# Optimization experiments

Hardware: AMD Instinct MI355X
Metric: run time of the kernel (lower is better)

## Reference

```python
import jax, jax.numpy as jnp
import numpy as np

D, H, L, N, BINS, V = 256, 8, 4, 512, 64, 20
DFF = 4 * D
DH = D // H
LAMBDA_RG = 10.0
STEPS = 10


def _lin(x, W, b):
    # torch nn.Linear convention: W is [out, in]
    return jnp.einsum('...i,oi->...o', x, W) + b


def _ln(x, g, b, eps=1e-5):
    m = x.mean(-1, keepdims=True)
    v = ((x - m) ** 2).mean(-1, keepdims=True)
    return (x - m) / jnp.sqrt(v + eps) * g + b


def _gelu(x):
    return jax.nn.gelu(x, approximate=False)  # torch nn.GELU default = exact erf


def _pos_encoding():
    pos = jnp.arange(N, dtype=jnp.float32)[:, None]
    div = jnp.exp(jnp.arange(0, D, 2, dtype=jnp.float32) * (-np.log(10000.0) / D))
    pe = jnp.zeros((N, D), jnp.float32)
    pe = pe.at[:, 0::2].set(jnp.sin(pos * div))
    pe = pe.at[:, 1::2].set(jnp.cos(pos * div))
    return pe


def _encoder_layer(x, Wqkv, bqkv, Wo, bo, g1, b1n, W1, b1, W2, b2, g2, b2n):
    # post-norm TransformerEncoderLayer, relu FFN, dropout=0 (eval)
    B, n, _ = x.shape
    qkv = _lin(x, Wqkv, bqkv)
    q, k, v = jnp.split(qkv, 3, axis=-1)
    hd = lambda t: t.reshape(B, n, H, DH).transpose(0, 2, 1, 3)
    q, k, v = hd(q), hd(k), hd(v)
    scores = jnp.einsum('bhqd,bhkd->bhqk', q, k) / jnp.sqrt(jnp.float32(DH))
    attn = jax.nn.softmax(scores, axis=-1)
    o = jnp.einsum('bhqk,bhkd->bhqd', attn, v).transpose(0, 2, 1, 3).reshape(B, n, D)
    x = _ln(x + _lin(o, Wo, bo), g1, b1n)
    ff = _lin(jax.nn.relu(_lin(x, W1, b1)), W2, b2)
    return _ln(x + ff, g2, b2n)


def setup_inputs() -> dict:
    key = jax.random.key(0)
    ks = list(jax.random.split(key, 24))
    it = iter(ks)
    w = lambda shape: jax.random.normal(next(it), shape, jnp.float32) * 0.02
    inp = {
        'tokens': jax.random.randint(next(it), (1, N), 0, V, dtype=jnp.int32),
        'noise': jax.random.normal(next(it), (1, N, 3), jnp.float32),
        'emb': w((V, D)),
        'Wqkv': w((L, 3 * D, D)), 'bqkv': jnp.zeros((L, 3 * D), jnp.float32),
        'Wo': w((L, D, D)), 'bo': jnp.zeros((L, D), jnp.float32),
        'ln1_g': jnp.ones((L, D), jnp.float32), 'ln1_b': jnp.zeros((L, D), jnp.float32),
        'W1': w((L, DFF, D)), 'b1': jnp.zeros((L, DFF), jnp.float32),
        'W2': w((L, D, DFF)), 'b2': jnp.zeros((L, D), jnp.float32),
        'ln2_g': jnp.ones((L, D), jnp.float32), 'ln2_b': jnp.zeros((L, D), jnp.float32),
        'aW1': w((D, D)), 'ab1': jnp.zeros((D,), jnp.float32),
        'aW2': w((1, D)), 'ab2': jnp.zeros((1,), jnp.float32),
        'cW': w((D, D)), 'cb': jnp.zeros((D,), jnp.float32),
        'dW1': w((D, 2 * D)), 'db1': jnp.zeros((D,), jnp.float32),
        'dW2': w((BINS, D)), 'db2': jnp.zeros((BINS,), jnp.float32),
        'tW1': w((D, D)), 'tb1': jnp.zeros((D,), jnp.float32),
        'tW2': w((2, D)), 'tb2': jnp.zeros((2,), jnp.float32),
        'pW': w((3, D)), 'pb': jnp.zeros((3,), jnp.float32),
    }
    return inp


def _forward(tokens, noise, emb, Wqkv, bqkv, Wo, bo, ln1_g, ln1_b, W1, b1, W2, b2,
             ln2_g, ln2_b, aW1, ab1, aW2, ab2, cW, cb, dW1, db1, dW2, db2,
             tW1, tb1, tW2, tb2, pW, pb):
    x = emb[tokens] + _pos_encoding()[None]  # [1,N,D]
    for l in range(L):
        x = _encoder_layer(x, Wqkv[l], bqkv[l], Wo[l], bo[l], ln1_g[l], ln1_b[l],
                           W1[l], b1[l], W2[l], b2[l], ln2_g[l], ln2_b[l])
    # AdaptiveAlphaPredictor
    a = jax.nn.sigmoid(_lin(_gelu(_lin(x, aW1, ab1)), aW2, ab2))
    alpha = (1.2 + a * (3.5 - 1.2))[..., 0]  # [1,N]
    # CSOCKernelAttention: distance power-law * exp-decay kernel
    idx = jnp.arange(N, dtype=jnp.float32)
    r = jnp.abs(idx[:, None] - idx[None, :]) + 1e-4  # [N,N]
    alpha_pair = (alpha[..., :, None] + alpha[..., None, :]) * 0.5  # [1,N,N]
    kernel = r[None] ** (-alpha_pair) * jnp.exp(-r[None] / LAMBDA_RG)
    kernel = kernel / (kernel.sum(-1, keepdims=True) + 1e-8)
    latent = jnp.einsum('bij,bjd->bid', kernel, x)
    # ContactPriorHead
    h = _lin(latent, cW, cb)
    contact = jax.nn.sigmoid(jnp.einsum('bid,bjd->bij', h, h))
    # DistogramHead: expand+concat+MLP (memory-bound O(N^2 d))
    xi = jnp.broadcast_to(latent[:, :, None, :], (1, N, N, D))
    xj = jnp.broadcast_to(latent[:, None, :, :], (1, N, N, D))
    pair = jnp.concatenate([xi, xj], axis=-1)  # [1,N,N,2D]
    disto = _lin(_gelu(_lin(pair, dW1, db1)), dW2, db2)  # [1,N,N,BINS]
    # TorsionGenerator
    t = _lin(_gelu(_lin(latent, tW1, tb1)), tW2, tb2)
    phi = jnp.tanh(t[..., 0]) * np.pi
    psi = jnp.tanh(t[..., 1]) * np.pi
    # DiffusionCoordinateInitializer (STEPS is a small fixed constant)
    target = _lin(latent, pW, pb)  # [1,N,3]
    c = noise
    for step in reversed(range(STEPS)):
        a_t = (step + 1) / STEPS
        c = a_t * c + (1.0 - a_t) * target
    return latent, alpha, contact, disto, phi, psi, c


def reference(tokens, noise, emb, Wqkv, bqkv, Wo, bo, ln1_g, ln1_b, W1, b1, W2, b2,
              ln2_g, ln2_b, aW1, ab1, aW2, ab2, cW, cb, dW1, db1, dW2, db2,
              tW1, tb1, tW2, tb2, pW, pb):
    return _forward(tokens, noise, emb, Wqkv, bqkv, Wo, bo, ln1_g, ln1_b, W1, b1,
                    W2, b2, ln2_g, ln2_b, aW1, ab1, aW2, ab2, cW, cb, dW1, db1,
                    dW2, db2, tW1, tb1, tW2, tb2, pW, pb)
```

## Files before the change

### kernel.cpp

```cpp
#include <hip/hip_runtime.h>
#include <hip/hip_bf16.h>

typedef __attribute__((ext_vector_type(8))) short bf16x8;
typedef __attribute__((ext_vector_type(4))) float f32x4;
typedef unsigned short ushort;

#define OFF_QKV 0
#define OFF_WO  786432
#define OFF_W1  1048576
#define OFF_W2  2097152
#define OFF_AW1 3145728
#define OFF_CW  3211264
#define OFF_DW1 3276800
#define OFF_TW1 3407872
#define WB_TOTAL 3473408

__device__ inline float gelu_f(float x) {
    return 0.5f * x * (1.0f + erff(x * 0.70710678118654752f));
}

__device__ inline ushort f2bfu(float x) {
    __hip_bfloat16 b = __float2bfloat16(x);
    return *reinterpret_cast<ushort*>(&b);
}

__device__ inline uint4 pack_bf8(float4 a, float4 b) {
    uint4 p;
    p.x = f2bfu(a.x) | ((unsigned)f2bfu(a.y) << 16);
    p.y = f2bfu(a.z) | ((unsigned)f2bfu(a.w) << 16);
    p.z = f2bfu(b.x) | ((unsigned)f2bfu(b.y) << 16);
    p.w = f2bfu(b.z) | ((unsigned)f2bfu(b.w) << 16);
    return p;
}

__device__ inline float wave_sum(float v) {
#pragma unroll
    for (int o = 32; o > 0; o >>= 1) v += __shfl_xor(v, o);
    return v;
}
__device__ inline float wave_max(float v) {
#pragma unroll
    for (int o = 32; o > 0; o >>= 1) v = fmaxf(v, __shfl_xor(v, o));
    return v;
}

__global__ void convw_k(const float* __restrict__ Wqkv, const float* __restrict__ Wo,
                        const float* __restrict__ W1, const float* __restrict__ W2,
                        const float* __restrict__ aW1, const float* __restrict__ cW,
                        const float* __restrict__ dW1, const float* __restrict__ tW1,
                        ushort* __restrict__ dst) {
    size_t i = ((size_t)blockIdx.x * 256 + threadIdx.x) * 8;
    if (i >= WB_TOTAL) return;
    const float* src;
    size_t off;
    if (i < OFF_WO)        { src = Wqkv; off = i; }
    else if (i < OFF_W1)   { src = Wo;   off = i - OFF_WO; }
    else if (i < OFF_W2)   { src = W1;   off = i - OFF_W1; }
    else if (i < OFF_AW1)  { src = W2;   off = i - OFF_W2; }
    else if (i < OFF_CW)   { src = aW1;  off = i - OFF_AW1; }
    else if (i < OFF_DW1)  { src = cW;   off = i - OFF_CW; }
    else if (i < OFF_TW1)  { src = dW1;  off = i - OFF_DW1; }
    else                   { src = tW1;  off = i - OFF_TW1; }
    float4 f0 = *(const float4*)&src[off];
    float4 f1 = *(const float4*)&src[off + 4];
    *(uint4*)&dst[i] = pack_bf8(f0, f1);
}

__global__ void embed_k(const int* __restrict__ tokens, const float* __restrict__ emb,
                        float* __restrict__ x, ushort* __restrict__ xb) {
    int n = blockIdx.x, t = threadIdx.x;
    float e = emb[(size_t)tokens[n] * 256 + t];
    int k = t >> 1;
    float div = expf((float)(2 * k) * (-9.210340371976184f / 256.0f));
    float arg = (float)n * div;
    float v = e + ((t & 1) ? cosf(arg) : sinf(arg));
    x[(size_t)n * 256 + t] = v;
    xb[(size_t)n * 256 + t] = f2bfu(v);
}

template <int ACT, int OBF>
__global__ __launch_bounds__(256) void gemm_bf(const ushort* __restrict__ A,
                                               const ushort* __restrict__ Wb,
                                               const float* __restrict__ bias,
                                               float* __restrict__ C,
                                               ushort* __restrict__ Cb,
                                               int Nn, int K, int lda, int ldw, int koff,
                                               size_t woff, size_t boff) {
    __shared__ ushort Al[2][2048];
    __shared__ ushort Wl[2][2048];
    const int t = threadIdx.x;
    const int bm = blockIdx.y * 64, bn = blockIdx.x * 64;
    const int lane = t & 63, wv = t >> 6;
    const int lo = lane & 15, hi = lane >> 4;

    const ushort* aptr = A + (size_t)(bm + lane) * lda + wv * 8;
    const ushort* wptr = Wb + woff + (size_t)(bn + lane) * ldw + koff + wv * 8;

    f32x4 acc0 = {0.f, 0.f, 0.f, 0.f}, acc1 = acc0, acc2 = acc0, acc3 = acc0;
    uint4 a = *(const uint4*)aptr;
    uint4 w = *(const uint4*)wptr;
    const int nsteps = K >> 5;
    for (int s = 0; s < nsteps; ++s) {
        const int buf = s & 1;
        *(uint4*)&Al[buf][t * 8] = a;
        *(uint4*)&Wl[buf][t * 8] = w;
        __syncthreads();
        if (s + 1 < nsteps) {
            a = *(const uint4*)(aptr + (s + 1) * 32);
            w = *(const uint4*)(wptr + (s + 1) * 32);
        }
        bf16x8 af = *(bf16x8*)&Al[buf][(hi * 64 + wv * 16 + lo) * 8];
        bf16x8 b0 = *(bf16x8*)&Wl[buf][(hi * 64 + 0 + lo) * 8];
        bf16x8 b1 = *(bf16x8*)&Wl[buf][(hi * 64 + 16 + lo) * 8];
        bf16x8 b2 = *(bf16x8*)&Wl[buf][(hi * 64 + 32 + lo) * 8];
        bf16x8 b3 = *(bf16x8*)&Wl[buf][(hi * 64 + 48 + lo) * 8];
        acc0 = __builtin_amdgcn_mfma_f32_16x16x32_bf16(af, b0, acc0, 0, 0, 0);
        acc1 = __builtin_amdgcn_mfma_f32_16x16x32_bf16(af, b1, acc1, 0, 0, 0);
        acc2 = __builtin_amdgcn_mfma_f32_16x16x32_bf16(af, b2, acc2, 0, 0, 0);
        acc3 = __builtin_amdgcn_mfma_f32_16x16x32_bf16(af, b3, acc3, 0, 0, 0);
    }

    float bv0 = bias ? bias[boff + bn + 0 + lo] : 0.0f;
    float bv1 = bias ? bias[boff + bn + 16 + lo] : 0.0f;
    float bv2 = bias ? bias[boff + bn + 32 + lo] : 0.0f;
    float bv3 = bias ? bias[boff + bn + 48 + lo] : 0.0f;
#pragma unroll
    for (int r = 0; r < 4; ++r) {
        size_t rw = (size_t)(bm + wv * 16 + hi * 4 + r) * Nn + bn;
        float v0 = acc0[r] + bv0, v1 = acc1[r] + bv1, v2 = acc2[r] + bv2, v3 = acc3[r] + bv3;
        if (ACT == 1) {
            v0 = fmaxf(v0, 0.f); v1 = fmaxf(v1, 0.f); v2 = fmaxf(v2, 0.f); v3 = fmaxf(v3, 0.f);
        }
        if (ACT == 2) {
            v0 = gelu_f(v0); v1 = gelu_f(v1); v2 = gelu_f(v2); v3 = gelu_f(v3);
        }
        if (OBF) {
            Cb[rw + 0 + lo] = f2bfu(v0);
            Cb[rw + 16 + lo] = f2bfu(v1);
            Cb[rw + 32 + lo] = f2bfu(v2);
            Cb[rw + 48 + lo] = f2bfu(v3);
        } else {
            C[rw + 0 + lo] = v0;
            C[rw + 16 + lo] = v1;
            C[rw + 32 + lo] = v2;
            C[rw + 48 + lo] = v3;
        }
    }
}

__global__ __launch_bounds__(256) void heads_k(const ushort* __restrict__ A,
                                               const ushort* __restrict__ Wb,
                                               const float* __restrict__ cb,
                                               const float* __restrict__ db1,
                                               const float* __restrict__ tb1,
                                               float* __restrict__ hbuf,
                                               float* __restrict__ U,
                                               float* __restrict__ Vv,
                                               float* __restrict__ t1t) {
    size_t woff; int ldw, koff, act; const float* bias; float* C;
    const int z = blockIdx.z;
    if (z == 0)      { woff = OFF_CW;  ldw = 256; koff = 0;   bias = cb;      act = 0; C = hbuf; }
    else if (z == 1) { woff = OFF_DW1; ldw = 512; koff = 0;   bias = db1;     act = 0; C = U; }
    else if (z == 2) { woff = OFF_DW1; ldw = 512; koff = 256; bias = nullptr; act = 0; C = Vv; }
    else             { woff = OFF_TW1; ldw = 256; koff = 0;   bias = tb1;     act = 2; C = t1t; }

    __shared__ ushort Al[2][2048];
    __shared__ ushort Wl[2][2048];
    const int t = threadIdx.x;
    const int bm = blockIdx.y * 64, bn = blockIdx.x * 64;
    const int lane = t & 63, wv = t >> 6;
    const int lo = lane & 15, hi = lane >> 4;

    const ushort* aptr = A + (size_t)(bm + lane) * 256 + wv * 8;
    const ushort* wptr = Wb + woff + (size_t)(bn + lane) * ldw + koff + wv * 8;

    f32x4 acc0 = {0.f, 0.f, 0.f, 0.f}, acc1 = acc0, acc2 = acc0, acc3 = acc0;
    uint4 a = *(const uint4*)aptr;
    uint4 w = *(const uint4*)wptr;
    for (int s = 0; s < 8; ++s) {
        const int buf = s & 1;
        *(uint4*)&Al[buf][t * 8] = a;
        *(uint4*)&Wl[buf][t * 8] = w;
        __syncthreads();
        if (s < 7) {
            a = *(const uint4*)(aptr + (s + 1) * 32);
            w = *(const uint4*)(wptr + (s + 1) * 32);
        }
        bf16x8 af = *(bf16x8*)&Al[buf][(hi * 64 + wv * 16 + lo) * 8];
        bf16x8 b0 = *(bf16x8*)&Wl[buf][(hi * 64 + 0 + lo) * 8];
        bf16x8 b1 = *(bf16x8*)&Wl[buf][(hi * 64 + 16 + lo) * 8];
        bf16x8 b2 = *(bf16x8*)&Wl[buf][(hi * 64 + 32 + lo) * 8];
        bf16x8 b3 = *(bf16x8*)&Wl[buf][(hi * 64 + 48 + lo) * 8];
        acc0 = __builtin_amdgcn_mfma_f32_16x16x32_bf16(af, b0, acc0, 0, 0, 0);
        acc1 = __builtin_amdgcn_mfma_f32_16x16x32_bf16(af, b1, acc1, 0, 0, 0);
        acc2 = __builtin_amdgcn_mfma_f32_16x16x32_bf16(af, b2, acc2, 0, 0, 0);
        acc3 = __builtin_amdgcn_mfma_f32_16x16x32_bf16(af, b3, acc3, 0, 0, 0);
    }

    float bv0 = bias ? bias[bn + 0 + lo] : 0.0f;
    float bv1 = bias ? bias[bn + 16 + lo] : 0.0f;
    float bv2 = bias ? bias[bn + 32 + lo] : 0.0f;
    float bv3 = bias ? bias[bn + 48 + lo] : 0.0f;
#pragma unroll
    for (int r = 0; r < 4; ++r) {
        size_t rw = (size_t)(bm + wv * 16 + hi * 4 + r) * 256 + bn;
        float v0 = acc0[r] + bv0, v1 = acc1[r] + bv1, v2 = acc2[r] + bv2, v3 = acc3[r] + bv3;
        if (act == 2) { v0 = gelu_f(v0); v1 = gelu_f(v1); v2 = gelu_f(v2); v3 = gelu_f(v3); }
        C[rw + 0 + lo] = v0;
        C[rw + 16 + lo] = v1;
        C[rw + 32 + lo] = v2;
        C[rw + 48 + lo] = v3;
    }
}

__global__ __launch_bounds__(256) void attn_k(const float* __restrict__ qkv,
                                              ushort* __restrict__ ob) {
    __shared__ float sc[4][512];
    int t = threadIdx.x;
    int w = t >> 6, lane = t & 63;
    int q = blockIdx.x * 4 + w;
    int h = blockIdx.y;
    const float* qptr = qkv + (size_t)q * 768 + h * 32;
    const float* kbase = qkv + 256 + h * 32;
    const float* vbase = qkv + 512 + h * 32;
    float qv[32];
#pragma unroll
    for (int d = 0; d < 32; d += 4) {
        float4 f = *(const float4*)(qptr + d);
        qv[d] = f.x; qv[d + 1] = f.y; qv[d + 2] = f.z; qv[d + 3] = f.w;
    }
    float mx = -1e30f;
    for (int k = lane; k < 512; k += 64) {
        const float* kp = kbase + (size_t)k * 768;
        float s = 0.0f;
#pragma unroll
        for (int d = 0; d < 32; d += 4) {
            float4 f = *(const float4*)(kp + d);
            s = fmaf(qv[d], f.x, s); s = fmaf(qv[d + 1], f.y, s);
            s = fmaf(qv[d + 2], f.z, s); s = fmaf(qv[d + 3], f.w, s);
        }
        s *= 0.17677669529663687f;
        sc[w][k] = s;
        mx = fmaxf(mx, s);
    }
    mx = wave_max(mx);
    float sum = 0.0f;
    for (int k = lane; k < 512; k += 64) {
        float e = expf(sc[w][k] - mx);
        sc[w][k] = e;
        sum += e;
    }
    sum = wave_sum(sum);
    float inv = 1.0f / sum;
    __syncthreads();
    int d = lane & 31, half = lane >> 5;
    const float* vp = vbase + d;
    const int kb = half * 256;
    float a0 = 0.f, a1 = 0.f, a2 = 0.f, a3 = 0.f;
    float a4 = 0.f, a5 = 0.f, a6 = 0.f, a7 = 0.f;
    for (int k = kb; k < kb + 256; k += 8) {
        float4 p0 = *(const float4*)&sc[w][k];
        float4 p1 = *(const float4*)&sc[w][k + 4];
        a0 = fmaf(p0.x, vp[(size_t)(k + 0) * 768], a0);
        a1 = fmaf(p0.y, vp[(size_t)(k + 1) * 768], a1);
        a2 = fmaf(p0.z, vp[(size_t)(k + 2) * 768], a2);
        a3 = fmaf(p0.w, vp[(size_t)(k + 3) * 768], a3);
        a4 = fmaf(p1.x, vp[(size_t)(k + 4) * 768], a4);
        a5 = fmaf(p1.y, vp[(size_t)(k + 5) * 768], a5);
        a6 = fmaf(p1.z, vp[(size_t)(k + 6) * 768], a6);
        a7 = fmaf(p1.w, vp[(size_t)(k + 7) * 768], a7);
    }
    float accv = ((a0 + a1) + (a2 + a3)) + ((a4 + a5) + (a6 + a7));
    accv += __shfl_down(accv, 32);
    if (lane < 32) ob[(size_t)q * 256 + h * 32 + d] = f2bfu(accv * inv);
}

__global__ void ln_res_k(float* __restrict__ x, const float* __restrict__ y,
                         const float* __restrict__ g, const float* __restrict__ b,
                         size_t goff, ushort* __restrict__ xb) {
    int row = blockIdx.x, t = threadIdx.x;
    __shared__ float red[8];
    float v = x[row * 256 + t] + y[row * 256 + t];
    float s = wave_sum(v);
    if ((t & 63) == 0) red[t >> 6] = s;
    __syncthreads();
    float mean = (red[0] + red[1] + red[2] + red[3]) * (1.0f / 256.0f);
    float d = v - mean;
    float s2 = wave_sum(d * d);
    if ((t & 63) == 0) red[4 + (t >> 6)] = s2;
    __syncthreads();
    float var = (red[4] + red[5] + red[6] + red[7]) * (1.0f / 256.0f);
    float res = d * rsqrtf(var + 1e-5f) * g[goff + t] + b[goff + t];
    x[row * 256 + t] = res;
    xb[row * 256 + t] = f2bfu(res);
}

__global__ void alpha_k(const float* __restrict__ t1, const float* __restrict__ aW2,
                        const float* __restrict__ ab2, float* __restrict__ alphaf,
                        float* __restrict__ out_alpha) {
    int t = threadIdx.x, w = t >> 6, lane = t & 63;
    int n = blockIdx.x * 4 + w;
    const float* r = t1 + (size_t)n * 256;
    float s = 0.0f;
    for (int d = lane; d < 256; d += 64) s = fmaf(r[d], aW2[d], s);
    s = wave_sum(s);
    if (lane == 0) {
        float z = s + ab2[0];
        float a = 1.0f / (1.0f + expf(-z));
        float al = 1.2f + 2.3f * a;
        alphaf[n] = al;
        out_alpha[n] = al;
    }
}

__global__ void csock_k(const float* __restrict__ x, const float* __restrict__ alphaf,
                        float* __restrict__ latent, float* __restrict__ out_latent,
                        ushort* __restrict__ latentb) {
    int i = blockIdx.x, t = threadIdx.x;
    __shared__ float wgt[512];
    __shared__ float red[4];
    float ai = alphaf[i];
    float lsum = 0.0f;
    for (int j = t; j < 512; j += 256) {
        float r = fabsf((float)(i - j)) + 1e-4f;
        float ap = 0.5f * (ai + alphaf[j]);
        float wv = powf(r, -ap) * expf(-r * 0.1f);
        wgt[j] = wv;
        lsum += wv;
    }
    float s = wave_sum(lsum);
    if ((t & 63) == 0) red[t >> 6] = s;
    __syncthreads();
    float S = red[0] + red[1] + red[2] + red[3] + 1e-8f;
    float acc = 0.0f;
    for (int j = 0; j < 512; ++j) acc = fmaf(wgt[j], x[(size_t)j * 256 + t], acc);
    float res = acc / S;
    latent[(size_t)i * 256 + t] = res;
    out_latent[(size_t)i * 256 + t] = res;
    latentb[(size_t)i * 256 + t] = f2bfu(res);
}

__global__ __launch_bounds__(256) void finals_k(const float* __restrict__ h,
                                                const float* __restrict__ t1t,
                                                const float* __restrict__ latentf,
                                                const float* __restrict__ tW2,
                                                const float* __restrict__ tb2,
                                                const float* __restrict__ pW,
                                                const float* __restrict__ pb,
                                                const float* __restrict__ noise,
                                                float* __restrict__ out_contact,
                                                float* __restrict__ phi,
                                                float* __restrict__ psi,
                                                float* __restrict__ outc) {
    const int blk = blockIdx.x;
    const int t = threadIdx.x;
    if (blk < 512) {
        int i = blk;
        __shared__ float hi_s[256];
        hi_s[t] = h[(size_t)i * 256 + t];
        __syncthreads();
        for (int j = t; j < 512; j += 256) {
            const float* hj = h + (size_t)j * 256;
            float s = 0.0f;
#pragma unroll 4
            for (int d = 0; d < 256; d += 4) {
                float4 a = *(const float4*)&hi_s[d];
                float4 b = *(const float4*)&hj[d];
                s = fmaf(a.x, b.x, s); s = fmaf(a.y, b.y, s);
                s = fmaf(a.z, b.z, s); s = fmaf(a.w, b.w, s);
            }
            out_contact[(size_t)i * 512 + j] = 1.0f / (1.0f + expf(-s));
        }
    } else if (blk < 640) {
        int w = t >> 6, lane = t & 63;
        int n = (blk - 512) * 4 + w;
        const float* r = t1t + (size_t)n * 256;
        float s0 = 0.0f, s1 = 0.0f;
        for (int d = lane; d < 256; d += 64) {
            float v = r[d];
            s0 = fmaf(v, tW2[d], s0);
            s1 = fmaf(v, tW2[256 + d], s1);
        }
        s0 = wave_sum(s0);
        s1 = wave_sum(s1);
        if (lane == 0) {
            phi[n] = tanhf(s0 + tb2[0]) * 3.14159265358979323846f;
            psi[n] = tanhf(s1 + tb2[1]) * 3.14159265358979323846f;
        }
    } else {
        int idx = (blk - 640) * 256 + t;
        if (idx >= 512 * 3) return;
        int n = idx / 3, a = idx % 3;
        const float* r = latentf + (size_t)n * 256;
        float s = pb[a];
        for (int d = 0; d < 256; ++d) s = fmaf(r[d], pW[(size_t)a * 256 + d], s);
        float c = noise[idx];
#pragma unroll
        for (int st = 9; st >= 0; --st) {
            float at = (float)(st + 1) * 0.1f;
            c = at * c + (1.0f - at) * s;
        }
        outc[idx] = c;
    }
}

__global__ __launch_bounds__(256) void disto_k(const float* __restrict__ U,
                                               const float* __restrict__ V,
                                               const float* __restrict__ dW2,
                                               const float* __restrict__ db2,
                                               float* __restrict__ out) {
    __shared__ short hsl[32 * 64 * 8];
    __shared__ short w2l[32 * 64 * 8];
    const int t = threadIdx.x;
    const int i = blockIdx.x;
    const int row = t >> 2;
    const int dq = t & 3;

#pragma unroll
    for (int c = 0; c < 8; ++c) {
        int dblk = dq * 8 + c;
        int d0 = dblk * 8;
        float4 w0 = *(const float4*)&dW2[(size_t)row * 256 + d0];
        float4 w1 = *(const float4*)&dW2[(size_t)row * 256 + d0 + 4];
        *(uint4*)&w2l[(dblk * 64 + row) * 8] = pack_bf8(w0, w1);
    }

    const int wv = t >> 6, lane = t & 63;
    const int lo = lane & 15, hi = lane >> 4;
    const int jw = wv * 16;
    float dbv[4];
#pragma unroll
    for (int nt = 0; nt < 4; ++nt) dbv[nt] = db2[nt * 16 + lo];

    for (int p = 0; p < 8; ++p) {
        const int j0 = p * 64;
#pragma unroll
        for (int c = 0; c < 8; ++c) {
            int dblk = dq * 8 + c;
            int d0 = dblk * 8;
            float4 u0 = *(const float4*)&U[(size_t)i * 256 + d0];
            float4 u1 = *(const float4*)&U[(size_t)i * 256 + d0 + 4];
            float4 v0 = *(const float4*)&V[(size_t)(j0 + row) * 256 + d0];
            float4 v1 = *(const float4*)&V[(size_t)(j0 + row) * 256 + d0 + 4];
            float4 h0, h1;
            h0.x = gelu_f(u0.x + v0.x); h0.y = gelu_f(u0.y + v0.y);
            h0.z = gelu_f(u0.z + v0.z); h0.w = gelu_f(u0.w + v0.w);
            h1.x = gelu_f(u1.x + v1.x); h1.y = gelu_f(u1.y + v1.y);
            h1.z = gelu_f(u1.z + v1.z); h1.w = gelu_f(u1.w + v1.w);
            *(uint4*)&hsl[(dblk * 64 + row) * 8] = pack_bf8(h0, h1);
        }
        __syncthreads();

        f32x4 acc0 = {0.f, 0.f, 0.f, 0.f}, acc1 = acc0, acc2 = acc0, acc3 = acc0;
#pragma unroll
        for (int kk = 0; kk < 8; ++kk) {
            int db = kk * 4 + hi;
            bf16x8 a = *(bf16x8*)&hsl[(db * 64 + jw + lo) * 8];
            bf16x8 b0 = *(bf16x8*)&w2l[(db * 64 + 0 + lo) * 8];
            bf16x8 b1 = *(bf16x8*)&w2l[(db * 64 + 16 + lo) * 8];
            bf16x8 b2 = *(bf16x8*)&w2l[(db * 64 + 32 + lo) * 8];
            bf16x8 b3 = *(bf16x8*)&w2l[(db * 64 + 48 + lo) * 8];
            acc0 = __builtin_amdgcn_mfma_f32_16x16x32_bf16(a, b0, acc0, 0, 0, 0);
            acc1 = __builtin_amdgcn_mfma_f32_16x16x32_bf16(a, b1, acc1, 0, 0, 0);
            acc2 = __builtin_amdgcn_mfma_f32_16x16x32_bf16(a, b2, acc2, 0, 0, 0);
            acc3 = __builtin_amdgcn_mfma_f32_16x16x32_bf16(a, b3, acc3, 0, 0, 0);
        }
#pragma unroll
        for (int r = 0; r < 4; ++r) {
            size_t jg = (size_t)i * 512 + j0 + jw + hi * 4 + r;
            out[jg * 64 + 0 + lo] = acc0[r] + dbv[0];
            out[jg * 64 + 16 + lo] = acc1[r] + dbv[1];
            out[jg * 64 + 32 + lo] = acc2[r] + dbv[2];
            out[jg * 64 + 48 + lo] = acc3[r] + dbv[3];
        }
        __syncthreads();
    }
}

extern "C" void kernel_launch(void* const* d_in, const int* in_sizes, int n_in,
                              void* d_out, int out_size, void* d_ws, size_t ws_size,
                              hipStream_t stream) {
    const int* tokens  = (const int*)d_in[0];
    const float* noise = (const float*)d_in[1];
    const float* emb   = (const float*)d_in[2];
    const float* Wqkv  = (const float*)d_in[3];
    const float* bqkv  = (const float*)d_in[4];
    const float* Wo    = (const float*)d_in[5];
    const float* bo    = (const float*)d_in[6];
    const float* ln1_g = (const float*)d_in[7];
    const float* ln1_b = (const float*)d_in[8];
    const float* W1    = (const float*)d_in[9];
    const float* b1    = (const float*)d_in[10];
    const float* W2    = (const float*)d_in[11];
    const float* b2    = (const float*)d_in[12];
    const float* ln2_g = (const float*)d_in[13];
    const float* ln2_b = (const float*)d_in[14];
    const float* aW1   = (const float*)d_in[15];
    const float* ab1   = (const float*)d_in[16];
    const float* aW2   = (const float*)d_in[17];
    const float* ab2   = (const float*)d_in[18];
    const float* cW    = (const float*)d_in[19];
    const float* cb    = (const float*)d_in[20];
    const float* dW1   = (const float*)d_in[21];
    const float* db1   = (const float*)d_in[22];
    const float* dW2   = (const float*)d_in[23];
    const float* db2   = (const float*)d_in[24];
    const float* tW1   = (const float*)d_in[25];
    const float* tb1   = (const float*)d_in[26];
    const float* tW2   = (const float*)d_in[27];
    const float* tb2   = (const float*)d_in[28];
    const float* pW    = (const float*)d_in[29];
    const float* pb    = (const float*)d_in[30];

    float* out         = (float*)d_out;
    float* out_latent  = out;
    float* out_alpha   = out + 131072;
    float* out_contact = out + 131584;
    float* out_disto   = out + 393728;
    float* out_phi     = out + 17170944;
    float* out_psi     = out + 17171456;
    float* out_c       = out + 17171968;

    float* scratch = out_disto;
    float* x    = scratch;
    float* qkv  = scratch + 131072;
    float* t1t  = scratch + 655360;
    float* y    = scratch + 1179648;
    float* hbuf = scratch + 1310720;
    float* t1a  = scratch + 1441792;
    ushort* wb      = (ushort*)(scratch + 2000000);
    ushort* xb      = (ushort*)(scratch + 3740000);
    ushort* ob      = (ushort*)(scratch + 3810000);
    ushort* ffhb    = (ushort*)(scratch + 3880000);
    ushort* latentb = (ushort*)(scratch + 4150000);

    float* latentf = (float*)d_ws;
    float* U       = latentf + 131072;
    float* Vv      = U + 131072;
    float* alphaf  = Vv + 131072;

    convw_k<<<1696, 256, 0, stream>>>(Wqkv, Wo, W1, W2, aW1, cW, dW1, tW1, wb);
    embed_k<<<512, 256, 0, stream>>>(tokens, emb, x, xb);

    for (int l = 0; l < 4; ++l) {
        gemm_bf<0, 0><<<dim3(12, 8), 256, 0, stream>>>(xb, wb, bqkv, qkv, nullptr,
                                                       768, 256, 256, 256, 0,
                                                       OFF_QKV + (size_t)l * 196608, (size_t)l * 768);
        attn_k<<<dim3(128, 8), 256, 0, stream>>>(qkv, ob);
        gemm_bf<0, 0><<<dim3(4, 8), 256, 0, stream>>>(ob, wb, bo, y, nullptr,
                                                      256, 256, 256, 256, 0,
                                                      OFF_WO + (size_t)l * 65536, (size_t)l * 256);
        ln_res_k<<<512, 256, 0, stream>>>(x, y, ln1_g, ln1_b, (size_t)l * 256, xb);
        gemm_bf<1, 1><<<dim3(16, 8), 256, 0, stream>>>(xb, wb, b1, nullptr, ffhb,
                                                       1024, 256, 256, 256, 0,
                                                       OFF_W1 + (size_t)l * 262144, (size_t)l * 1024);
        gemm_bf<0, 0><<<dim3(4, 8), 256, 0, stream>>>(ffhb, wb, b2, y, nullptr,
                                                      256, 1024, 1024, 1024, 0,
                                                      OFF_W2 + (size_t)l * 262144, (size_t)l * 256);
        ln_res_k<<<512, 256, 0, stream>>>(x, y, ln2_g, ln2_b, (size_t)l * 256, xb);
    }

    gemm_bf<2, 0><<<dim3(4, 8), 256, 0, stream>>>(xb, wb, ab1, t1a, nullptr,
                                                  256, 256, 256, 256, 0, OFF_AW1, 0);
    alpha_k<<<128, 256, 0, stream>>>(t1a, aW2, ab2, alphaf, out_alpha);

    csock_k<<<512, 256, 0, stream>>>(x, alphaf, latentf, out_latent, latentb);

    heads_k<<<dim3(4, 8, 4), 256, 0, stream>>>(latentb, wb, cb, db1, tb1,
                                               hbuf, U, Vv, t1t);

    finals_k<<<646, 256, 0, stream>>>(hbuf, t1t, latentf, tW2, tb2, pW, pb, noise,
                                      out_contact, out_phi, out_psi, out_c);

    disto_k<<<512, 256, 0, stream>>>(U, Vv, dW2, db2, out_disto);
}
```

Measured before the change: 487.3 us.

## Split-K the FFN2 GEMM and split disto pairwise kernel across more blocks

The second FFN GEMM (K=1024) previously ran on only 32 blocks. It is replaced by a 4-way split-K kernel with double-buffered LDS, and its partial sums are reduced inside a new residual+LayerNorm kernel that also adds the bias. The disto kernel is also split along j into two halves per row, which doubles the grid, halves the per-block hidden tile, and adds an XOR swizzle to the LDS layout to reduce bank conflicts. The cost is extra partial-sum traffic, the dW2 conversion being repeated in twice as many blocks, and a new scratch region placed inside the disto output area.

```diff
diff --git a/kernel.cpp b/kernel.cpp
--- a/kernel.cpp
+++ b/kernel.cpp
@@ -146,6 +146,78 @@
             C[rw + 48 + lo] = v3;
         }
     }
+}
+
+__global__ __launch_bounds__(256) void ffn2_splitk(const ushort* __restrict__ A,
+                                                   const ushort* __restrict__ Wb,
+                                                   float* __restrict__ yp,
+                                                   size_t woff) {
+    __shared__ ushort Al[2][2048];
+    __shared__ ushort Wl[2][2048];
+    const int t = threadIdx.x;
+    const int bm = blockIdx.y * 64, bn = blockIdx.x * 64;
+    const int ks = blockIdx.z;
+    const int lane = t & 63, wv = t >> 6;
+    const int lo = lane & 15, hi = lane >> 4;
+
+    const ushort* aptr = A + (size_t)(bm + lane) * 1024 + ks * 256 + wv * 8;
+    const ushort* wptr = Wb + woff + (size_t)(bn + lane) * 1024 + ks * 256 + wv * 8;
+
+    f32x4 acc0 = {0.f, 0.f, 0.f, 0.f}, acc1 = acc0, acc2 = acc0, acc3 = acc0;
+    uint4 a = *(const uint4*)aptr;
+    uint4 w = *(const uint4*)wptr;
+    for (int s = 0; s < 8; ++s) {
+        const int buf = s & 1;
+        *(uint4*)&Al[buf][t * 8] = a;
+        *(uint4*)&Wl[buf][t * 8] = w;
+        __syncthreads();
+        if (s < 7) {
+            a = *(const uint4*)(aptr + (s + 1) * 32);
+            w = *(const uint4*)(wptr + (s + 1) * 32);
+        }
+        bf16x8 af = *(bf16x8*)&Al[buf][(hi * 64 + wv * 16 + lo) * 8];
+        bf16x8 b0 = *(bf16x8*)&Wl[buf][(hi * 64 + 0 + lo) * 8];
+        bf16x8 b1 = *(bf16x8*)&Wl[buf][(hi * 64 + 16 + lo) * 8];
+        bf16x8 b2 = *(bf16x8*)&Wl[buf][(hi * 64 + 32 + lo) * 8];
+        bf16x8 b3 = *(bf16x8*)&Wl[buf][(hi * 64 + 48 + lo) * 8];
+        acc0 = __builtin_amdgcn_mfma_f32_16x16x32_bf16(af, b0, acc0, 0, 0, 0);
+        acc1 = __builtin_amdgcn_mfma_f32_16x16x32_bf16(af, b1, acc1, 0, 0, 0);
+        acc2 = __builtin_amdgcn_mfma_f32_16x16x32_bf16(af, b2, acc2, 0, 0, 0);
+        acc3 = __builtin_amdgcn_mfma_f32_16x16x32_bf16(af, b3, acc3, 0, 0, 0);
+    }
+
+    float* yo = yp + (size_t)ks * 131072;
+#pragma unroll
+    for (int r = 0; r < 4; ++r) {
+        size_t rw = (size_t)(bm + wv * 16 + hi * 4 + r) * 256 + bn;
+        yo[rw + 0 + lo] = acc0[r];
+        yo[rw + 16 + lo] = acc1[r];
+        yo[rw + 32 + lo] = acc2[r];
+        yo[rw + 48 + lo] = acc3[r];
+    }
+}
+
+__global__ void ln_res4_k(float* __restrict__ x, const float* __restrict__ yp,
+                          const float* __restrict__ b2, size_t b2off,
+                          const float* __restrict__ g, const float* __restrict__ b,
+                          size_t goff, ushort* __restrict__ xb) {
+    int row = blockIdx.x, t = threadIdx.x;
+    __shared__ float red[8];
+    size_t idx = (size_t)row * 256 + t;
+    float v = x[idx] + ((yp[idx] + yp[idx + 131072]) + (yp[idx + 262144] + yp[idx + 393216]))
+            + b2[b2off + t];
+    float s = wave_sum(v);
+    if ((t & 63) == 0) red[t >> 6] = s;
+    __syncthreads();
+    float mean = (red[0] + red[1] + red[2] + red[3]) * (1.0f / 256.0f);
+    float d = v - mean;
+    float s2 = wave_sum(d * d);
+    if ((t & 63) == 0) red[4 + (t >> 6)] = s2;
+    __syncthreads();
+    float var = (red[4] + red[5] + red[6] + red[7]) * (1.0f / 256.0f);
+    float res = d * rsqrtf(var + 1e-5f) * g[goff + t] + b[goff + t];
+    x[idx] = res;
+    xb[idx] = f2bfu(res);
 }
 
 __global__ __launch_bounds__(256) void heads_k(const ushort* __restrict__ A,
@@ -409,69 +481,66 @@
                                                const float* __restrict__ dW2,
                                                const float* __restrict__ db2,
                                                float* __restrict__ out) {
-    __shared__ short hsl[32 * 64 * 8];
+    __shared__ short hsl[32 * 32 * 8];
     __shared__ short w2l[32 * 64 * 8];
     const int t = threadIdx.x;
     const int i = blockIdx.x;
-    const int row = t >> 2;
-    const int dq = t & 3;
-
-#pragma unroll
-    for (int c = 0; c < 8; ++c) {
-        int dblk = dq * 8 + c;
-        int d0 = dblk * 8;
-        float4 w0 = *(const float4*)&dW2[(size_t)row * 256 + d0];
-        float4 w1 = *(const float4*)&dW2[(size_t)row * 256 + d0 + 4];
-        *(uint4*)&w2l[(dblk * 64 + row) * 8] = pack_bf8(w0, w1);
-    }
-
-    const int wv = t >> 6, lane = t & 63;
-    const int lo = lane & 15, hi = lane >> 4;
-    const int jw = wv * 16;
-    float dbv[4];
-#pragma unroll
-    for (int nt = 0; nt < 4; ++nt) dbv[nt] = db2[nt * 16 + lo];
-
-    for (int p = 0; p < 8; ++p) {
-        const int j0 = p * 64;
+    const int jhalf = blockIdx.y;
+
+    {
+        const int brow = t >> 2, dq = t & 3;
 #pragma unroll
         for (int c = 0; c < 8; ++c) {
             int dblk = dq * 8 + c;
             int d0 = dblk * 8;
+            float4 w0 = *(const float4*)&dW2[(size_t)brow * 256 + d0];
+            float4 w1 = *(const float4*)&dW2[(size_t)brow * 256 + d0 + 4];
+            *(uint4*)&w2l[(dblk * 64 + brow) * 8] = pack_bf8(w0, w1);
+        }
+    }
+
+    const int wv = t >> 6, lane = t & 63;
+    const int lo = lane & 15, hi = lane >> 4;
+    const int jt = wv & 1, bh = wv >> 1;
+    float dbv0 = db2[(bh * 2 + 0) * 16 + lo];
+    float dbv1 = db2[(bh * 2 + 1) * 16 + lo];
+
+    const int jrow = t & 31, dg = t >> 5;
+
+    for (int p = 0; p < 8; ++p) {
+        const int j0 = jhalf * 256 + p * 32;
+#pragma unroll
+        for (int c = 0; c < 4; ++c) {
+            int dblk = dg * 4 + c;
+            int d0 = dblk * 8;
             float4 u0 = *(const float4*)&U[(size_t)i * 256 + d0];
             float4 u1 = *(const float4*)&U[(size_t)i * 256 + d0 + 4];
-            float4 v0 = *(const float4*)&V[(size_t)(j0 + row) * 256 + d0];
-            float4 v1 = *(const float4*)&V[(size_t)(j0 + row) * 256 + d0 + 4];
+            float4 v0 = *(const float4*)&V[(size_t)(j0 + jrow) * 256 + d0];
+            float4 v1 = *(const float4*)&V[(size_t)(j0 + jrow) * 256 + d0 + 4];
             float4 h0, h1;
             h0.x = gelu_f(u0.x + v0.x); h0.y = gelu_f(u0.y + v0.y);
             h0.z = gelu_f(u0.z + v0.z); h0.w = gelu_f(u0.w + v0.w);
             h1.x = gelu_f(u1.x + v1.x); h1.y = gelu_f(u1.y + v1.y);
             h1.z = gelu_f(u1.z + v1.z); h1.w = gelu_f(u1.w + v1.w);
-            *(uint4*)&hsl[(dblk * 64 + row) * 8] = pack_bf8(h0, h1);
+            *(uint4*)&hsl[(dblk * 32 + (jrow ^ dblk)) * 8] = pack_bf8(h0, h1);
         }
         __syncthreads();
 
-        f32x4 acc0 = {0.f, 0.f, 0.f, 0.f}, acc1 = acc0, acc2 = acc0, acc3 = acc0;
+        f32x4 acc0 = {0.f, 0.f, 0.f, 0.f}, acc1 = acc0;
 #pragma unroll
         for (int kk = 0; kk < 8; ++kk) {
             int db = kk * 4 + hi;
-            bf16x8 a = *(bf16x8*)&hsl[(db * 64 + jw + lo) * 8];
-            bf16x8 b0 = *(bf16x8*)&w2l[(db * 64 + 0 + lo) * 8];
-            bf16x8 b1 = *(bf16x8*)&w2l[(db * 64 + 16 + lo) * 8];
-            bf16x8 b2 = *(bf16x8*)&w2l[(db * 64 + 32 + lo) * 8];
-            bf16x8 b3 = *(bf16x8*)&w2l[(db * 64 + 48 + lo) * 8];
+            bf16x8 a = *(bf16x8*)&hsl[(db * 32 + ((jt * 16 + lo) ^ db)) * 8];
+            bf16x8 b0 = *(bf16x8*)&w2l[(db * 64 + (bh * 2 + 0) * 16 + lo) * 8];
+            bf16x8 b1 = *(bf16x8*)&w2l[(db * 64 + (bh * 2 + 1) * 16 + lo) * 8];
             acc0 = __builtin_amdgcn_mfma_f32_16x16x32_bf16(a, b0, acc0, 0, 0, 0);
             acc1 = __builtin_amdgcn_mfma_f32_16x16x32_bf16(a, b1, acc1, 0, 0, 0);
-            acc2 = __builtin_amdgcn_mfma_f32_16x16x32_bf16(a, b2, acc2, 0, 0, 0);
-            acc3 = __builtin_amdgcn_mfma_f32_16x16x32_bf16(a, b3, acc3, 0, 0, 0);
         }
 #pragma unroll
         for (int r = 0; r < 4; ++r) {
-            size_t jg = (size_t)i * 512 + j0 + jw + hi * 4 + r;
-            out[jg * 64 + 0 + lo] = acc0[r] + dbv[0];
-            out[jg * 64 + 16 + lo] = acc1[r] + dbv[1];
-            out[jg * 64 + 32 + lo] = acc2[r] + dbv[2];
-            out[jg * 64 + 48 + lo] = acc3[r] + dbv[3];
+            size_t jg = (size_t)i * 512 + j0 + jt * 16 + hi * 4 + r;
+            out[jg * 64 + (bh * 2 + 0) * 16 + lo] = acc0[r] + dbv0;
+            out[jg * 64 + (bh * 2 + 1) * 16 + lo] = acc1[r] + dbv1;
         }
         __syncthreads();
     }
@@ -533,6 +602,7 @@
     ushort* ob      = (ushort*)(scratch + 3810000);
     ushort* ffhb    = (ushort*)(scratch + 3880000);
     ushort* latentb = (ushort*)(scratch + 4150000);
+    float* yp   = scratch + 4300000;
 
     float* latentf = (float*)d_ws;
     float* U       = latentf + 131072;
@@ -554,10 +624,10 @@
         gemm_bf<1, 1><<<dim3(16, 8), 256, 0, stream>>>(xb, wb, b1, nullptr, ffhb,
                                                        1024, 256, 256, 256, 0,
                                                        OFF_W1 + (size_t)l * 262144, (size_t)l * 1024);
-        gemm_bf<0, 0><<<dim3(4, 8), 256, 0, stream>>>(ffhb, wb, b2, y, nullptr,
-                                                      256, 1024, 1024, 1024, 0,
-                                                      OFF_W2 + (size_t)l * 262144, (size_t)l * 256);
-        ln_res_k<<<512, 256, 0, stream>>>(x, y, ln2_g, ln2_b, (size_t)l * 256, xb);
+        ffn2_splitk<<<dim3(4, 8, 4), 256, 0, stream>>>(ffhb, wb, yp,
+                                                       OFF_W2 + (size_t)l * 262144);
+        ln_res4_k<<<512, 256, 0, stream>>>(x, yp, b2, (size_t)l * 256,
+                                           ln2_g, ln2_b, (size_t)l * 256, xb);
     }
 
     gemm_bf<2, 0><<<dim3(4, 8), 256, 0, stream>>>(xb, wb, ab1, t1a, nullptr,
@@ -572,5 +642,5 @@
     finals_k<<<646, 256, 0, stream>>>(hbuf, t1t, latentf, tW2, tb2, pW, pb, noise,
                                       out_contact, out_phi, out_psi, out_c);
 
-    disto_k<<<512, 256, 0, stream>>>(U, Vv, dW2, db2, out_disto);
-}
+    disto_k<<<dim3(512, 2), 256, 0, stream>>>(U, Vv, dW2, db2, out_disto);
+}
```

Measured after the change: 452.1 us. 1.08x faster.
